# Optimization experiments

Hardware: AMD Instinct MI355X
Metric: run time of the kernel (lower is better)

The kernel has to match this reference:

```python
import jax, jax.numpy as jnp
import numpy as np

N_LAYERS = 11
DILATIONS = tuple(2 ** i for i in range(N_LAYERS))   # 1..1024
MEM_SIZES = DILATIONS                                 # kernel=2 -> 1 past tap -> mem = dilation
HOP = 128
C_SCALE = 1.0
FFT = 256       # channel width
NUM_CLS = 256   # mu-law classes
COND = 80       # mel bands
FRAMES = 16


def setup_inputs() -> dict:
    key = jax.random.key(0)
    ks = jax.random.split(key, 10)
    s = 0.05  # keep logits well-scaled for softmax sampling
    return {
        "y": jax.random.normal(ks[0], (COND, FRAMES), jnp.float32),
        "samples": jax.random.uniform(ks[1], (FRAMES * HOP,), jnp.float32),
        "emb_raw": jax.random.normal(ks[2], (NUM_CLS, FFT), jnp.float32) * 0.5,
        "condition_W": jax.random.normal(ks[3], (N_LAYERS * FFT, COND), jnp.float32) * s,
        "WV_past": jax.random.normal(ks[4], (N_LAYERS, FFT, FFT, 1), jnp.float32) * s,
        "WV_present": jax.random.normal(ks[5], (N_LAYERS, FFT, FFT), jnp.float32) * s,
        "W_o_w": jax.random.normal(ks[6], (N_LAYERS, FFT, FFT), jnp.float32) * s,
        "W_o_b": jax.random.normal(ks[7], (N_LAYERS, FFT), jnp.float32) * s,
        "end_w": jax.random.normal(ks[8], (NUM_CLS, FFT), jnp.float32) * s,
        "end_b": jax.random.normal(ks[9], (NUM_CLS,), jnp.float32) * s,
    }


def reference(y, samples, emb_raw, condition_W, WV_past, WV_present, W_o_w, W_o_b, end_w, end_b):
    emb = jnp.tanh(emb_raw)                      # fftnet.emb[0].weight.tanh()
    T = y.shape[1] * HOP
    # F.interpolate nearest with scale_factor=hop_length == frame repeat
    yu = jnp.repeat(y, HOP, axis=1)              # [COND, T]
    # precompute all conditioning projections (condition_W @ y[:, i], chunked per layer)
    conds = (condition_W @ yu).reshape(N_LAYERS, FFT, T).transpose(2, 0, 1)  # [T, L, FFT]

    bufs0 = tuple(jnp.zeros((FFT, m), jnp.float32) for m in MEM_SIZES)
    x0 = emb[NUM_CLS // 2 - 1]
    n_taps = WV_past.shape[3]

    def step(carry, inp):
        x, bufs = carry
        cond_t, u, t = inp
        new_bufs = []
        for j in range(N_LAYERS):
            mem = bufs[j]
            m = MEM_SIZES[j]
            idx = t % m                                   # ring-buffer write/oldest-read ptr
            h = cond_t[j]
            ii = idx
            for k in range(n_taps):                       # read past taps (before write)
                h = h + WV_past[j, :, :, k] @ mem[:, ii]
                ii = (ii + DILATIONS[j]) % m
            h = h + WV_present[j] @ x
            new_bufs.append(mem.at[:, idx].set(x))        # write current x into ring buffer
            h = jax.nn.relu(h)
            z = W_o_w[j] @ h + W_o_b[j]
            x = jax.nn.relu(z + x)                        # residual + relu
        logits = (end_w @ x + end_b) * C_SCALE
        cum = jnp.cumsum(jax.nn.softmax(logits))
        new_idx = jnp.argmax(cum > u)                     # nonzero(cum > u)[0]
        return (emb[new_idx], tuple(new_bufs)), new_idx

    ts = jnp.arange(T)
    _, outputs = jax.lax.scan(step, (x0, bufs0), (conds, samples, ts))
    return outputs  # [T] int sampled mu-law classes
```

## Files before the change

kernel.cpp:

```cpp
#include <hip/hip_runtime.h>
#include <math.h>


#define T_STEPS 2048
#define NROLE   32

typedef unsigned long long u64;
typedef float v64f __attribute__((ext_vector_type(64)));

#define OFF_EMBT   0
#define OFF_WPET   65536
#define OFF_WVPET  131072
#define OFF_RINGS  196608
#define OFF_TAPQ   1244672
#define OFF_ZQ     1408512
#define OFF_XQ     1419776
#define WS_FLOATS  1425408

#define FIDX     0
#define FBAR(r)  (32 + 32*(r))

__device__ __forceinline__ float ldc(const float* p) {
  int v = __hip_atomic_load((const int*)p, __ATOMIC_RELAXED, __HIP_MEMORY_SCOPE_AGENT);
  return __int_as_float(v);
}
__device__ __forceinline__ void stc(float* p, float x) {
  __hip_atomic_store((int*)p, __float_as_int(x), __ATOMIC_RELAXED, __HIP_MEMORY_SCOPE_AGENT);
}
__device__ __forceinline__ u64 ldq(const u64* p) {
  return __hip_atomic_load(p, __ATOMIC_RELAXED, __HIP_MEMORY_SCOPE_AGENT);
}
__device__ __forceinline__ void stq(u64* p, float v, int tag) {
  u64 x = (u64)(unsigned)__float_as_int(v) | ((u64)(unsigned)tag << 32);
  __hip_atomic_store(p, x, __ATOMIC_RELAXED, __HIP_MEMORY_SCOPE_AGENT);
}
__device__ __forceinline__ int ptag(u64 q) { return (int)(q >> 32); }
__device__ __forceinline__ float pval(u64 q) { return __int_as_float((int)(unsigned)q); }

__device__ __forceinline__ float spin_pair(const u64* p, int want) {
  int bud = 1 << 20; u64 q;
  do { q = ldq(p); } while (ptag(q) < want && --bud > 0);
  return pval(q);
}
__device__ __forceinline__ void spin3(const u64* p1, const u64* p2, const u64* p3,
                                      int want, float& v1, float& v2, float& v3) {
  int bud = 1 << 20; u64 q1, q2, q3; bool ok;
  do {
    q1 = ldq(p1); q2 = ldq(p2); q3 = ldq(p3);
    ok = (ptag(q1) >= want) & (ptag(q2) >= want) & (ptag(q3) >= want);
  } while (!ok && --bud > 0);
  v1 = pval(q1); v2 = pval(q2); v3 = pval(q3);
}
__device__ __forceinline__ void spin_tag2(const u64* p1, const u64* p2, int w1, int w2) {
  int bud = 1 << 20; u64 q1, q2; bool ok;
  do {
    q1 = ldq(p1); q2 = ldq(p2);
    ok = (ptag(q1) >= w1) & (ptag(q2) >= w2);
  } while (!ok && --bud > 0);
}
__device__ __forceinline__ void wait1(int* f, int want) {
  int it = 0;
  while (__hip_atomic_load(f, __ATOMIC_RELAXED, __HIP_MEMORY_SCOPE_AGENT) < want) {
    if (++it > (1 << 22)) break;
  }
  (void)__hip_atomic_load(f, __ATOMIC_ACQUIRE, __HIP_MEMORY_SCOPE_AGENT);
}
__device__ __forceinline__ void post(int* f, int v) {
  __hip_atomic_store(f, v, __ATOMIC_RELEASE, __HIP_MEMORY_SCOPE_AGENT);
}

__global__ __launch_bounds__(512, 1)
void fftnet_kernel(const float* __restrict__ y, const float* __restrict__ samples,
                   const float* __restrict__ emb_raw, const float* __restrict__ condW,
                   const float* __restrict__ WV_past, const float* __restrict__ WV_present,
                   const float* __restrict__ W_o_w, const float* __restrict__ W_o_b,
                   const float* __restrict__ end_w, const float* __restrict__ end_b,
                   int* __restrict__ out, float* __restrict__ ws)
{
  const int tid = threadIdx.x;
  const int role = blockIdx.x;
  int* iflags = (int*)(ws + WS_FLOATS);
  u64* zq  = (u64*)(ws + OFF_ZQ);
  u64* xq  = (u64*)(ws + OFF_XQ);
  u64* tq  = (u64*)(ws + OFF_TAPQ);

  __shared__ float s_x[256];
  __shared__ float s_h[256];
  __shared__ float s_p[1024];
  __shared__ float s_cond[16 * 256];
  __shared__ float s_tap[128];
  __shared__ float s_m[320];
  __shared__ unsigned long long s_mask[8];

  for (int i = role * 512 + tid; i < 65536; i += NROLE * 512)
    stc(ws + OFF_EMBT + i, tanhf(emb_raw[i]));
  __syncthreads();
  if (tid == 0) post(iflags + FBAR(role), 1);
  if (tid < NROLE) wait1(iflags + FBAR(tid), 1);
  __syncthreads();

  for (int n = role; n < 512; n += NROLE) {
    const float* wmat = (n < 256) ? WV_present : WV_past;
    int cls = n & 255;
    int c = tid & 255, s2 = tid >> 8;
    float acc = 0.f;
    for (int k = 128 * s2; k < 128 * s2 + 128; ++k)
      acc += wmat[c * 256 + k] * ws[OFF_EMBT + cls * 256 + k];
    s_p[s2 * 256 + c] = acc;
    __syncthreads();
    if (tid < 256)
      stc(ws + ((n < 256) ? OFF_WPET : OFF_WVPET) + cls * 256 + tid, s_p[tid] + s_p[256 + tid]);
    __syncthreads();
  }
  __syncthreads();
  if (tid == 0) post(iflags + FBAR(role), 2);
  if (tid < NROLE) wait1(iflags + FBAR(tid), 2);
  __syncthreads();
  __builtin_amdgcn_fence(__ATOMIC_ACQUIRE, "agent");
  __syncthreads();

  if (role == 0) {
    const int c = tid & 255, s2 = tid >> 8;
    v64f we0, we1;
#pragma unroll
    for (int i = 0; i < 64; ++i) we0[i] = end_w[c * 256 + 128 * s2 + i];
#pragma unroll
    for (int i = 0; i < 64; ++i) we1[i] = end_w[c * 256 + 128 * s2 + 64 + i];
    const float eb = end_b[c];
    const float b10 = W_o_b[10 * 256 + c];
    const u64* pza = zq + (10 * 2 + 0) * 256;
    const u64* pzb = zq + (10 * 2 + 1) * 256;
    const u64* pxq = xq + 10 * 256;
    const int lane = tid & 63, w = tid >> 6;
    if (tid == 0)
      __hip_atomic_store(iflags + FIDX, (1 << 8) | 127, __ATOMIC_RELAXED,
                         __HIP_MEMORY_SCOPE_AGENT);

    for (int t = 0; t < T_STEPS; ++t) {
      float u = samples[t];
      if (tid < 256) {
        float a, b, r3;
        spin3(pza + tid, pzb + tid, pxq + tid, t + 1, a, b, r3);
        s_x[tid] = fmaxf(a + b + b10 + r3, 0.f);
      }
      __syncthreads();
      float acc = 0.f;
#pragma unroll
      for (int i = 0; i < 64; ++i) acc += we0[i] * s_x[128 * s2 + i];
#pragma unroll
      for (int i = 0; i < 64; ++i) acc += we1[i] * s_x[128 * s2 + 64 + i];
      s_p[s2 * 256 + c] = acc;
      __syncthreads();
      float logit = 0.f;
      if (tid < 256) logit = s_p[tid] + s_p[256 + tid] + eb;
      float vmax = (tid < 256) ? logit : -3.4e38f;
#pragma unroll
      for (int d = 32; d > 0; d >>= 1) vmax = fmaxf(vmax, __shfl_xor(vmax, d, 64));
      if (lane == 0) s_m[280 + w] = vmax;
      __syncthreads();
      float mx = fmaxf(fmaxf(s_m[280], s_m[281]), fmaxf(s_m[282], s_m[283]));
      float e = (tid < 256) ? expf(logit - mx) : 0.f;
      float vs = e;
#pragma unroll
      for (int d = 32; d > 0; d >>= 1) vs += __shfl_xor(vs, d, 64);
      if (lane == 0) s_m[288 + w] = vs;
      __syncthreads();
      float ssum = s_m[288] + s_m[289] + s_m[290] + s_m[291];
      float p = (tid < 256) ? (e / ssum) : 0.f;
      float v = p;
#pragma unroll
      for (int d = 1; d < 64; d <<= 1) {
        float o = __shfl_up(v, (unsigned)d, 64);
        if (lane >= d) v += o;
      }
      if (tid < 256 && lane == 63) s_m[256 + w] = v;
      __syncthreads();
      float offs = 0.f;
      if (tid < 256) for (int k = 0; k < w; ++k) offs += s_m[256 + k];
      float cum = v + offs;
      unsigned long long msk = __ballot(tid < 256 && (cum > u));
      if (lane == 0) s_mask[w] = msk;
      __syncthreads();
      if (tid == 0) {
        int idx = 0;
        for (int k = 0; k < 4; ++k) {
          unsigned long long m2 = s_mask[k];
          if (m2) { idx = k * 64 + (int)__builtin_ctzll(m2); break; }
        }
        __hip_atomic_store(iflags + FIDX, ((t + 2) << 8) | idx, __ATOMIC_RELAXED,
                           __HIP_MEMORY_SCOPE_AGENT);
        out[t] = idx;
      }
      __syncthreads();
    }

  } else if (role == 1) {
    v64f wo00, wo01;
    { int c = tid & 255, s2 = tid >> 8;
#pragma unroll
      for (int i = 0; i < 64; ++i) wo00[i] = W_o_w[c * 256 + 128 * s2 + i];
#pragma unroll
      for (int i = 0; i < 64; ++i) wo01[i] = W_o_w[c * 256 + 128 * s2 + 64 + i]; }
    const float b0 = W_o_b[tid & 255];
    for (int e = tid; e < 4096; e += 512) {
      int f = e >> 8, r = e & 255;
      float a = 0.f;
      for (int q = 0; q < 80; ++q) a += condW[r * 80 + q] * y[q * 16 + f];
      s_cond[f * 256 + r] = a;
    }
    __syncthreads();
    u64* px1 = xq + 1 * 256;
    int pidx = 127;

    for (int t = 0; t < T_STEPS; ++t) {
      float tapv = 0.f;
      if (tid < 256 && t > 0) tapv = ws[OFF_WVPET + pidx * 256 + tid];
      int v, bud = 1 << 20;
      do {
        v = __hip_atomic_load(iflags + FIDX, __ATOMIC_RELAXED, __HIP_MEMORY_SCOPE_AGENT);
      } while (v < ((t + 1) << 8) && --bud > 0);
      const int idx = v & 255;
      if (tid < 256) {
        s_x[tid] = ws[OFF_EMBT + idx * 256 + tid];
        float hv = s_cond[(t >> 7) * 256 + tid] + ws[OFF_WPET + idx * 256 + tid] + tapv;
        s_h[tid] = fmaxf(hv, 0.f);
      }
      __syncthreads();
      {
        int c = tid & 255, s2 = tid >> 8;
        float a0 = 0.f, a1 = 0.f;
#pragma unroll
        for (int i = 0; i < 64; ++i) a0 += wo00[i] * s_h[128 * s2 + i];
#pragma unroll
        for (int i = 0; i < 64; ++i) a1 += wo01[i] * s_h[128 * s2 + 64 + i];
        s_p[s2 * 256 + c] = a0 + a1;
      }
      __syncthreads();
      if (tid < 256)
        stq(px1 + tid, fmaxf(s_p[tid] + s_p[256 + tid] + b0 + s_x[tid], 0.f), t + 1);
      pidx = idx;
    }

  } else if (role <= 21) {
    const int jj = (role <= 11) ? (role - 1) : (role - 11);
    const int side = (role <= 11) ? 0 : 1;
    const int base = side * 128;
    v64f wpv, wov;
    { const float* W = WV_present + jj * 65536;
      int r = tid & 127, s = tid >> 7;
#pragma unroll
      for (int i = 0; i < 64; ++i) wpv[i] = W[(base + r) * 256 + 64 * s + i]; }
    { const float* W = W_o_w + jj * 65536;
      int c = tid & 255, s2 = tid >> 8;
#pragma unroll
      for (int i = 0; i < 64; ++i) wov[i] = W[c * 256 + base + 64 * s2 + i]; }
    const float bprev = W_o_b[(jj - 1) * 256 + (tid & 255)];
    for (int e = tid; e < 2048; e += 512) {
      int f = e >> 7, rr = e & 127;
      float a = 0.f;
      for (int q = 0; q < 80; ++q) a += condW[(jj * 256 + base + rr) * 80 + q] * y[q * 16 + f];
      s_cond[f * 128 + rr] = a;
    }
    __syncthreads();
    const int dj = 1 << jj, maskj = 2 * dj - 1;
    float* ringj = ws + OFF_RINGS + 512 * (dj - 1);
    const u64* pza = zq + ((jj - 1) * 2 + 0) * 256;
    const u64* pzb = zq + ((jj - 1) * 2 + 1) * 256;
    const u64* pxp = xq + (jj - 1) * 256;
    u64* zout = zq + (jj * 2 + side) * 256;
    u64* xout = xq + jj * 256;
    const u64* ptap = tq + (jj - 1) * 32 * 256;

    for (int t = 0; t < T_STEPS; ++t) {
      const int want = t + 1;
      if (tid < 256) {
        float xv;
        if (jj == 1) {
          xv = spin_pair(xq + 1 * 256 + tid, want);
        } else {
          float a, b, r3;
          spin3(pza + tid, pzb + tid, pxp + tid, want, a, b, r3);
          xv = fmaxf(a + b + bprev + r3, 0.f);
        }
        s_x[tid] = xv;
        if (side == 0) {
          stc(ringj + (t & maskj) * 256 + tid, xv);
          if (jj >= 2) stq(xout + tid, xv, want);
        }
      } else if (tid < 384) {
        int l = tid - 256;
        s_tap[l] = spin_pair(ptap + (t & 31) * 256 + base + l, want);
      }
      __syncthreads();
      { int r = tid & 127, s = tid >> 7;
        float acc = 0.f;
#pragma unroll
        for (int i = 0; i < 64; ++i) acc += wpv[i] * s_x[64 * s + i];
        s_p[s * 128 + r] = acc; }
      __syncthreads();
      if (tid < 128) {
        int f = t >> 7;
        float hv = s_p[tid] + s_p[128 + tid] + s_p[256 + tid] + s_p[384 + tid]
                 + s_cond[f * 128 + tid] + s_tap[tid];
        s_h[tid] = fmaxf(hv, 0.f);
      }
      __syncthreads();
      { int cc = tid & 255, s2 = tid >> 8;
        float acc = 0.f;
#pragma unroll
        for (int i = 0; i < 64; ++i) acc += wov[i] * s_h[64 * s2 + i];
        s_p[s2 * 256 + cc] = acc; }
      __syncthreads();
      if (side == 0)
        __builtin_amdgcn_fence(__ATOMIC_RELEASE, "agent");
      if (tid < 256) stq(zout + tid, s_p[tid] + s_p[256 + tid], want);
    }

  } else {
    const int j = role - 21;
    const int dj = 1 << j, maskj = 2 * dj - 1;
    v64f wq0, wq1;
    { const float* W = WV_past + j * 65536;
      int r = tid & 255, s2 = tid >> 8;
#pragma unroll
      for (int i = 0; i < 64; ++i) wq0[i] = W[r * 256 + 128 * s2 + i];
#pragma unroll
      for (int i = 0; i < 64; ++i) wq1[i] = W[r * 256 + 128 * s2 + 64 + i]; }
    float* ringj = ws + OFF_RINGS + 512 * (dj - 1);
    u64* tapj = tq + (j - 1) * 32 * 256;
    const u64* pza = zq + (j * 2 + 0) * 256;
    const u64* pzb = zq + (j * 2 + 1) * 256;

    for (int t = 0; t < T_STEPS; ++t) {
      int wgA = (t >= dj) ? (t - dj + 1) : (t - 31);
      if (wgA < t - 31) wgA = t - 31;
      int wgB = t - 31;
      if (tid < 256 && (wgA >= 1 || wgB >= 1))
        spin_tag2(pza + tid, pzb + tid, wgA, wgB);
      float tapv = 0.f;
      if (t >= dj) {
        if (tid < 256) s_x[tid] = ldc(ringj + ((t - dj) & maskj) * 256 + tid);
        __syncthreads();
        int r = tid & 255, s2 = tid >> 8;
        float acc = 0.f;
#pragma unroll
        for (int i = 0; i < 64; ++i) acc += wq0[i] * s_x[128 * s2 + i];
#pragma unroll
        for (int i = 0; i < 64; ++i) acc += wq1[i] * s_x[128 * s2 + 64 + i];
        s_p[s2 * 256 + r] = acc;
        __syncthreads();
        if (tid < 256) tapv = s_p[tid] + s_p[256 + tid];
      }
      if (tid < 256) stq(tapj + (t & 31) * 256 + tid, tapv, t + 1);
      __syncthreads();
    }
  }
}

extern "C" void kernel_launch(void* const* d_in, const int* in_sizes, int n_in,
                              void* d_out, int out_size, void* d_ws, size_t ws_size,
                              hipStream_t stream) {
  const float* y       = (const float*)d_in[0];
  const float* samples = (const float*)d_in[1];
  const float* emb_raw = (const float*)d_in[2];
  const float* condW   = (const float*)d_in[3];
  const float* WV_past = (const float*)d_in[4];
  const float* WV_pres = (const float*)d_in[5];
  const float* W_o_w   = (const float*)d_in[6];
  const float* W_o_b   = (const float*)d_in[7];
  const float* end_w   = (const float*)d_in[8];
  const float* end_b   = (const float*)d_in[9];
  (void)in_sizes; (void)n_in; (void)out_size; (void)ws_size;
  hipLaunchKernelGGL(fftnet_kernel, dim3(NROLE), dim3(512), 0, stream,
                     y, samples, emb_raw, condW, WV_past, WV_pres,
                     W_o_w, W_o_b, end_w, end_b, (int*)d_out, (float*)d_ws);
}
```

Baseline: 55.18 ms.

## Split each layer across four blocks and fuse layer-0 output into layer-1 blocks

Raises the persistent grid from 32 to 53 blocks so that each residual layer's present-matvec and output-projection is split four ways across blocks instead of two, and each produces a quarter of the z partial sums. Layer 0 becomes two blocks that publish only z partials, and layer 1 computes x from those plus the embedding and the sampled index, which is now published through a tagged 64-bit queue. The aim is to shorten the per-step serial critical path by doing less work per block per layer. In exchange, every consumer must spin on more flag words, and inter-block traffic grows.

```diff
diff --git a/kernel.cpp b/kernel.cpp
--- a/kernel.cpp
+++ b/kernel.cpp
@@ -3,7 +3,7 @@
 
 
 #define T_STEPS 2048
-#define NROLE   32
+#define NBLK    53
 
 typedef unsigned long long u64;
 typedef float v64f __attribute__((ext_vector_type(64)));
@@ -13,12 +13,12 @@
 #define OFF_WVPET  131072
 #define OFF_RINGS  196608
 #define OFF_TAPQ   1244672
-#define OFF_ZQ     1408512
-#define OFF_XQ     1419776
-#define WS_FLOATS  1425408
-
-#define FIDX     0
-#define FBAR(r)  (32 + 32*(r))
+#define OFF_ZQ4    1408512
+#define OFF_XQ     1431040
+#define OFF_IDXQ   1436672
+#define WS_FLOATS  1436736
+
+#define FBAR(r)  (32*(r))
 
 __device__ __forceinline__ float ldc(const float* p) {
   int v = __hip_atomic_load((const int*)p, __ATOMIC_RELAXED, __HIP_MEMORY_SCOPE_AGENT);
@@ -41,6 +41,11 @@
   int bud = 1 << 20; u64 q;
   do { q = ldq(p); } while (ptag(q) < want && --bud > 0);
   return pval(q);
+}
+__device__ __forceinline__ int spin_idx(const u64* p, int want) {
+  int bud = 1 << 20; u64 q;
+  do { q = ldq(p); } while (ptag(q) < want && --bud > 0);
+  return __float_as_int(pval(q)) & 255;
 }
 __device__ __forceinline__ void spin3(const u64* p1, const u64* p2, const u64* p3,
                                       int want, float& v1, float& v2, float& v3) {
@@ -50,6 +55,17 @@
     ok = (ptag(q1) >= want) & (ptag(q2) >= want) & (ptag(q3) >= want);
   } while (!ok && --bud > 0);
   v1 = pval(q1); v2 = pval(q2); v3 = pval(q3);
+}
+__device__ __forceinline__ void spin5(const u64* p0, const u64* p1, const u64* p2,
+                                      const u64* p3, const u64* p4, int want,
+                                      float& v0, float& v1, float& v2, float& v3, float& v4) {
+  int bud = 1 << 20; u64 q0, q1, q2, q3, q4; bool ok;
+  do {
+    q0 = ldq(p0); q1 = ldq(p1); q2 = ldq(p2); q3 = ldq(p3); q4 = ldq(p4);
+    ok = (ptag(q0) >= want) & (ptag(q1) >= want) & (ptag(q2) >= want)
+       & (ptag(q3) >= want) & (ptag(q4) >= want);
+  } while (!ok && --bud > 0);
+  v0 = pval(q0); v1 = pval(q1); v2 = pval(q2); v3 = pval(q3); v4 = pval(q4);
 }
 __device__ __forceinline__ void spin_tag2(const u64* p1, const u64* p2, int w1, int w2) {
   int bud = 1 << 20; u64 q1, q2; bool ok;
@@ -78,28 +94,29 @@
                    int* __restrict__ out, float* __restrict__ ws)
 {
   const int tid = threadIdx.x;
-  const int role = blockIdx.x;
+  const int bid = blockIdx.x;
   int* iflags = (int*)(ws + WS_FLOATS);
-  u64* zq  = (u64*)(ws + OFF_ZQ);
-  u64* xq  = (u64*)(ws + OFF_XQ);
-  u64* tq  = (u64*)(ws + OFF_TAPQ);
+  u64* zq4  = (u64*)(ws + OFF_ZQ4);
+  u64* xq   = (u64*)(ws + OFF_XQ);
+  u64* tq   = (u64*)(ws + OFF_TAPQ);
+  u64* idxq = (u64*)(ws + OFF_IDXQ);
 
   __shared__ float s_x[256];
   __shared__ float s_h[256];
   __shared__ float s_p[1024];
-  __shared__ float s_cond[16 * 256];
-  __shared__ float s_tap[128];
+  __shared__ float s_cond[2048];
+  __shared__ float s_tap[64];
   __shared__ float s_m[320];
   __shared__ unsigned long long s_mask[8];
 
-  for (int i = role * 512 + tid; i < 65536; i += NROLE * 512)
+  for (int i = bid * 512 + tid; i < 65536; i += NBLK * 512)
     stc(ws + OFF_EMBT + i, tanhf(emb_raw[i]));
   __syncthreads();
-  if (tid == 0) post(iflags + FBAR(role), 1);
-  if (tid < NROLE) wait1(iflags + FBAR(tid), 1);
-  __syncthreads();
-
-  for (int n = role; n < 512; n += NROLE) {
+  if (tid == 0) post(iflags + FBAR(bid), 1);
+  if (tid < NBLK) wait1(iflags + FBAR(tid), 1);
+  __syncthreads();
+
+  for (int n = bid; n < 512; n += NBLK) {
     const float* wmat = (n < 256) ? WV_present : WV_past;
     int cls = n & 255;
     int c = tid & 255, s2 = tid >> 8;
@@ -113,13 +130,13 @@
     __syncthreads();
   }
   __syncthreads();
-  if (tid == 0) post(iflags + FBAR(role), 2);
-  if (tid < NROLE) wait1(iflags + FBAR(tid), 2);
+  if (tid == 0) post(iflags + FBAR(bid), 2);
+  if (tid < NBLK) wait1(iflags + FBAR(tid), 2);
   __syncthreads();
   __builtin_amdgcn_fence(__ATOMIC_ACQUIRE, "agent");
   __syncthreads();
 
-  if (role == 0) {
+  if (bid == 0) {
     const int c = tid & 255, s2 = tid >> 8;
     v64f we0, we1;
 #pragma unroll
@@ -128,20 +145,21 @@
     for (int i = 0; i < 64; ++i) we1[i] = end_w[c * 256 + 128 * s2 + 64 + i];
     const float eb = end_b[c];
     const float b10 = W_o_b[10 * 256 + c];
-    const u64* pza = zq + (10 * 2 + 0) * 256;
-    const u64* pzb = zq + (10 * 2 + 1) * 256;
+    const u64* pz0 = zq4 + (10 * 4 + 0) * 256;
+    const u64* pz1 = zq4 + (10 * 4 + 1) * 256;
+    const u64* pz2 = zq4 + (10 * 4 + 2) * 256;
+    const u64* pz3 = zq4 + (10 * 4 + 3) * 256;
     const u64* pxq = xq + 10 * 256;
     const int lane = tid & 63, w = tid >> 6;
-    if (tid == 0)
-      __hip_atomic_store(iflags + FIDX, (1 << 8) | 127, __ATOMIC_RELAXED,
-                         __HIP_MEMORY_SCOPE_AGENT);
+    if (tid == 0) stq(idxq, __int_as_float(127), 1);
 
     for (int t = 0; t < T_STEPS; ++t) {
       float u = samples[t];
       if (tid < 256) {
-        float a, b, r3;
-        spin3(pza + tid, pzb + tid, pxq + tid, t + 1, a, b, r3);
-        s_x[tid] = fmaxf(a + b + b10 + r3, 0.f);
+        float a, b, cc, d, r3;
+        spin5(pz0 + tid, pz1 + tid, pz2 + tid, pz3 + tid, pxq + tid, t + 1, a, b, cc, d, r3);
+        float s01 = a + b, s23 = cc + d;
+        s_x[tid] = fmaxf(s01 + s23 + b10 + r3, 0.f);
       }
       __syncthreads();
       float acc = 0.f;
@@ -155,23 +173,23 @@
       if (tid < 256) logit = s_p[tid] + s_p[256 + tid] + eb;
       float vmax = (tid < 256) ? logit : -3.4e38f;
 #pragma unroll
-      for (int d = 32; d > 0; d >>= 1) vmax = fmaxf(vmax, __shfl_xor(vmax, d, 64));
+      for (int d2 = 32; d2 > 0; d2 >>= 1) vmax = fmaxf(vmax, __shfl_xor(vmax, d2, 64));
       if (lane == 0) s_m[280 + w] = vmax;
       __syncthreads();
       float mx = fmaxf(fmaxf(s_m[280], s_m[281]), fmaxf(s_m[282], s_m[283]));
       float e = (tid < 256) ? expf(logit - mx) : 0.f;
       float vs = e;
 #pragma unroll
-      for (int d = 32; d > 0; d >>= 1) vs += __shfl_xor(vs, d, 64);
+      for (int d2 = 32; d2 > 0; d2 >>= 1) vs += __shfl_xor(vs, d2, 64);
       if (lane == 0) s_m[288 + w] = vs;
       __syncthreads();
       float ssum = s_m[288] + s_m[289] + s_m[290] + s_m[291];
       float p = (tid < 256) ? (e / ssum) : 0.f;
       float v = p;
 #pragma unroll
-      for (int d = 1; d < 64; d <<= 1) {
-        float o = __shfl_up(v, (unsigned)d, 64);
-        if (lane >= d) v += o;
+      for (int d2 = 1; d2 < 64; d2 <<= 1) {
+        float o = __shfl_up(v, (unsigned)d2, 64);
+        if (lane >= d2) v += o;
       }
       if (tid < 256 && lane == 63) s_m[256 + w] = v;
       __syncthreads();
@@ -187,87 +205,82 @@
           unsigned long long m2 = s_mask[k];
           if (m2) { idx = k * 64 + (int)__builtin_ctzll(m2); break; }
         }
-        __hip_atomic_store(iflags + FIDX, ((t + 2) << 8) | idx, __ATOMIC_RELAXED,
-                           __HIP_MEMORY_SCOPE_AGENT);
+        stq(idxq, __int_as_float(idx), t + 2);
         out[t] = idx;
       }
       __syncthreads();
     }
 
-  } else if (role == 1) {
-    v64f wo00, wo01;
-    { int c = tid & 255, s2 = tid >> 8;
-#pragma unroll
-      for (int i = 0; i < 64; ++i) wo00[i] = W_o_w[c * 256 + 128 * s2 + i];
-#pragma unroll
-      for (int i = 0; i < 64; ++i) wo01[i] = W_o_w[c * 256 + 128 * s2 + 64 + i]; }
-    const float b0 = W_o_b[tid & 255];
-    for (int e = tid; e < 4096; e += 512) {
-      int f = e >> 8, r = e & 255;
-      float a = 0.f;
-      for (int q = 0; q < 80; ++q) a += condW[r * 80 + q] * y[q * 16 + f];
-      s_cond[f * 256 + r] = a;
-    }
-    __syncthreads();
-    u64* px1 = xq + 1 * 256;
-    int pidx = 127;
-
-    for (int t = 0; t < T_STEPS; ++t) {
-      float tapv = 0.f;
-      if (tid < 256 && t > 0) tapv = ws[OFF_WVPET + pidx * 256 + tid];
-      int v, bud = 1 << 20;
-      do {
-        v = __hip_atomic_load(iflags + FIDX, __ATOMIC_RELAXED, __HIP_MEMORY_SCOPE_AGENT);
-      } while (v < ((t + 1) << 8) && --bud > 0);
-      const int idx = v & 255;
-      if (tid < 256) {
-        s_x[tid] = ws[OFF_EMBT + idx * 256 + tid];
-        float hv = s_cond[(t >> 7) * 256 + tid] + ws[OFF_WPET + idx * 256 + tid] + tapv;
-        s_h[tid] = fmaxf(hv, 0.f);
-      }
-      __syncthreads();
-      {
-        int c = tid & 255, s2 = tid >> 8;
-        float a0 = 0.f, a1 = 0.f;
-#pragma unroll
-        for (int i = 0; i < 64; ++i) a0 += wo00[i] * s_h[128 * s2 + i];
-#pragma unroll
-        for (int i = 0; i < 64; ++i) a1 += wo01[i] * s_h[128 * s2 + 64 + i];
-        s_p[s2 * 256 + c] = a0 + a1;
-      }
-      __syncthreads();
-      if (tid < 256)
-        stq(px1 + tid, fmaxf(s_p[tid] + s_p[256 + tid] + b0 + s_x[tid], 0.f), t + 1);
-      pidx = idx;
-    }
-
-  } else if (role <= 21) {
-    const int jj = (role <= 11) ? (role - 1) : (role - 11);
-    const int side = (role <= 11) ? 0 : 1;
-    const int base = side * 128;
-    v64f wpv, wov;
-    { const float* W = WV_present + jj * 65536;
-      int r = tid & 127, s = tid >> 7;
-#pragma unroll
-      for (int i = 0; i < 64; ++i) wpv[i] = W[(base + r) * 256 + 64 * s + i]; }
-    { const float* W = W_o_w + jj * 65536;
-      int c = tid & 255, s2 = tid >> 8;
-#pragma unroll
-      for (int i = 0; i < 64; ++i) wov[i] = W[c * 256 + base + 64 * s2 + i]; }
-    const float bprev = W_o_b[(jj - 1) * 256 + (tid & 255)];
+  } else if (bid <= 2) {
+    const int side = bid - 1;
+    const int row = tid & 255, chunk = tid >> 8;
+    v64f wv;
+#pragma unroll
+    for (int i = 0; i < 64; ++i)
+      wv[i] = W_o_w[row * 256 + side * 128 + chunk * 64 + i];
     for (int e = tid; e < 2048; e += 512) {
       int f = e >> 7, rr = e & 127;
       float a = 0.f;
-      for (int q = 0; q < 80; ++q) a += condW[(jj * 256 + base + rr) * 80 + q] * y[q * 16 + f];
+      for (int q = 0; q < 80; ++q) a += condW[(side * 128 + rr) * 80 + q] * y[q * 16 + f];
       s_cond[f * 128 + rr] = a;
+    }
+    __syncthreads();
+    u64* zout = zq4 + (0 * 4 + side) * 256;
+    int pidx = 127;
+
+    for (int t = 0; t < T_STEPS; ++t) {
+      int idx = pidx;
+      if (tid < 128) {
+        float tapv = (t > 0) ? ws[OFF_WVPET + pidx * 256 + side * 128 + tid] : 0.f;
+        idx = spin_idx(idxq, t + 1);
+        float hv = s_cond[(t >> 7) * 128 + tid]
+                 + ws[OFF_WPET + idx * 256 + side * 128 + tid] + tapv;
+        s_h[tid] = fmaxf(hv, 0.f);
+        if (tid == 0) s_m[300] = __int_as_float(idx);
+      }
+      __syncthreads();
+      float acc = 0.f;
+#pragma unroll
+      for (int i = 0; i < 64; ++i) acc += wv[i] * s_h[64 * chunk + i];
+      s_p[chunk * 256 + row] = acc;
+      __syncthreads();
+      if (tid < 256) stq(zout + tid, s_p[tid] + s_p[256 + tid], t + 1);
+      pidx = (tid < 128) ? idx : __float_as_int(s_m[300]);
+      __syncthreads();
+    }
+
+  } else if (bid <= 42) {
+    const int jj = 1 + ((bid - 3) >> 2);
+    const int k  = (bid - 3) & 3;
+    v64f wv;
+    if (tid < 256) {
+      int r = tid & 63, s = tid >> 6;
+#pragma unroll
+      for (int i = 0; i < 64; ++i)
+        wv[i] = WV_present[jj * 65536 + (64 * k + r) * 256 + 64 * s + i];
+    } else {
+      int row = tid - 256;
+#pragma unroll
+      for (int i = 0; i < 64; ++i)
+        wv[i] = W_o_w[jj * 65536 + row * 256 + 64 * k + i];
+    }
+    const float bprev = W_o_b[(jj - 1) * 256 + (tid & 255)];
+    for (int e = tid; e < 1024; e += 512) {
+      int f = e >> 6, rr = e & 63;
+      float a = 0.f;
+      for (int q = 0; q < 80; ++q)
+        a += condW[(jj * 256 + 64 * k + rr) * 80 + q] * y[q * 16 + f];
+      s_cond[f * 64 + rr] = a;
     }
     __syncthreads();
     const int dj = 1 << jj, maskj = 2 * dj - 1;
     float* ringj = ws + OFF_RINGS + 512 * (dj - 1);
-    const u64* pza = zq + ((jj - 1) * 2 + 0) * 256;
-    const u64* pzb = zq + ((jj - 1) * 2 + 1) * 256;
+    const u64* pz0 = zq4 + ((jj - 1) * 4 + 0) * 256;
+    const u64* pz1 = zq4 + ((jj - 1) * 4 + 1) * 256;
+    const u64* pz2 = zq4 + ((jj - 1) * 4 + 2) * 256;
+    const u64* pz3 = zq4 + ((jj - 1) * 4 + 3) * 256;
     const u64* pxp = xq + (jj - 1) * 256;
-    u64* zout = zq + (jj * 2 + side) * 256;
+    u64* zout = zq4 + (jj * 4 + k) * 256;
     u64* xout = xq + jj * 256;
     const u64* ptap = tq + (jj - 1) * 32 * 256;
 
@@ -276,67 +289,73 @@
       if (tid < 256) {
         float xv;
         if (jj == 1) {
-          xv = spin_pair(xq + 1 * 256 + tid, want);
+          float a, b, iv;
+          spin3(pz0 + tid, pz1 + tid, idxq, want, a, b, iv);
+          int idx = __float_as_int(iv) & 255;
+          xv = fmaxf((a + b) + bprev + ws[OFF_EMBT + idx * 256 + tid], 0.f);
         } else {
-          float a, b, r3;
-          spin3(pza + tid, pzb + tid, pxp + tid, want, a, b, r3);
-          xv = fmaxf(a + b + bprev + r3, 0.f);
+          float a, b, cc, d, xp;
+          spin5(pz0 + tid, pz1 + tid, pz2 + tid, pz3 + tid, pxp + tid, want, a, b, cc, d, xp);
+          float s01 = a + b, s23 = cc + d;
+          xv = fmaxf(s01 + s23 + bprev + xp, 0.f);
         }
         s_x[tid] = xv;
-        if (side == 0) {
-          stc(ringj + (t & maskj) * 256 + tid, xv);
-          if (jj >= 2) stq(xout + tid, xv, want);
-        }
-      } else if (tid < 384) {
-        int l = tid - 256;
-        s_tap[l] = spin_pair(ptap + (t & 31) * 256 + base + l, want);
-      }
-      __syncthreads();
-      { int r = tid & 127, s = tid >> 7;
+        if (k == 0) stq(xout + tid, xv, want);
+      } else if (tid >= 384 && tid < 448) {
+        int l = tid - 384;
+        s_tap[l] = spin_pair(ptap + (t & 31) * 256 + 64 * k + l, want);
+      }
+      __syncthreads();
+      if (tid < 256) {
+        int r = tid & 63, s = tid >> 6;
         float acc = 0.f;
 #pragma unroll
-        for (int i = 0; i < 64; ++i) acc += wpv[i] * s_x[64 * s + i];
-        s_p[s * 128 + r] = acc; }
-      __syncthreads();
-      if (tid < 128) {
-        int f = t >> 7;
-        float hv = s_p[tid] + s_p[128 + tid] + s_p[256 + tid] + s_p[384 + tid]
-                 + s_cond[f * 128 + tid] + s_tap[tid];
+        for (int i = 0; i < 64; ++i) acc += wv[i] * s_x[64 * s + i];
+        s_p[s * 64 + r] = acc;
+      } else if (k == 0) {
+        int row = tid - 256;
+        stc(ringj + (t & maskj) * 256 + row, s_x[row]);
+      }
+      __syncthreads();
+      if (tid < 64) {
+        float hv = s_p[tid] + s_p[64 + tid] + s_p[128 + tid] + s_p[192 + tid]
+                 + s_cond[(t >> 7) * 64 + tid] + s_tap[tid];
         s_h[tid] = fmaxf(hv, 0.f);
       }
       __syncthreads();
-      { int cc = tid & 255, s2 = tid >> 8;
+      if (tid >= 256) {
+        int row = tid - 256;
         float acc = 0.f;
 #pragma unroll
-        for (int i = 0; i < 64; ++i) acc += wov[i] * s_h[64 * s2 + i];
-        s_p[s2 * 256 + cc] = acc; }
-      __syncthreads();
-      if (side == 0)
-        __builtin_amdgcn_fence(__ATOMIC_RELEASE, "agent");
-      if (tid < 256) stq(zout + tid, s_p[tid] + s_p[256 + tid], want);
+        for (int i = 0; i < 64; ++i) acc += wv[i] * s_h[i];
+        if (k == 0)
+          __builtin_amdgcn_fence(__ATOMIC_RELEASE, "agent");
+        stq(zout + row, acc, want);
+      }
+      __syncthreads();
     }
 
   } else {
-    const int j = role - 21;
+    const int j = bid - 42;
     const int dj = 1 << j, maskj = 2 * dj - 1;
     v64f wq0, wq1;
-    { const float* W = WV_past + j * 65536;
-      int r = tid & 255, s2 = tid >> 8;
-#pragma unroll
-      for (int i = 0; i < 64; ++i) wq0[i] = W[r * 256 + 128 * s2 + i];
-#pragma unroll
-      for (int i = 0; i < 64; ++i) wq1[i] = W[r * 256 + 128 * s2 + 64 + i]; }
+    { int r = tid & 255, s2 = tid >> 8;
+#pragma unroll
+      for (int i = 0; i < 64; ++i) wq0[i] = WV_past[j * 65536 + r * 256 + 128 * s2 + i];
+#pragma unroll
+      for (int i = 0; i < 64; ++i) wq1[i] = WV_past[j * 65536 + r * 256 + 128 * s2 + 64 + i]; }
     float* ringj = ws + OFF_RINGS + 512 * (dj - 1);
     u64* tapj = tq + (j - 1) * 32 * 256;
-    const u64* pza = zq + (j * 2 + 0) * 256;
-    const u64* pzb = zq + (j * 2 + 1) * 256;
+    const u64* z0 = zq4 + (j * 4 + 0) * 256;
 
     for (int t = 0; t < T_STEPS; ++t) {
-      int wgA = (t >= dj) ? (t - dj + 1) : (t - 31);
-      if (wgA < t - 31) wgA = t - 31;
-      int wgB = t - 31;
-      if (tid < 256 && (wgA >= 1 || wgB >= 1))
-        spin_tag2(pza + tid, pzb + tid, wgA, wgB);
+      int g0 = t - 31;
+      if (t >= dj && t - dj + 1 > g0) g0 = t - dj + 1;
+      int gk = t - 31;
+      if (tid < 256 && (g0 >= 1 || gk >= 1)) {
+        const u64* zk = zq4 + (j * 4 + (tid >> 6)) * 256;
+        spin_tag2(z0 + tid, zk + tid, g0, gk);
+      }
       float tapv = 0.f;
       if (t >= dj) {
         if (tid < 256) s_x[tid] = ldc(ringj + ((t - dj) & maskj) * 256 + tid);
@@ -371,7 +390,7 @@
   const float* end_w   = (const float*)d_in[8];
   const float* end_b   = (const float*)d_in[9];
   (void)in_sizes; (void)n_in; (void)out_size; (void)ws_size;
-  hipLaunchKernelGGL(fftnet_kernel, dim3(NROLE), dim3(512), 0, stream,
+  hipLaunchKernelGGL(fftnet_kernel, dim3(NBLK), dim3(512), 0, stream,
                      y, samples, emb_raw, condW, WV_past, WV_pres,
                      W_o_w, W_o_b, end_w, end_b, (int*)d_out, (float*)d_ws);
 }
```

Result: faster. 50.48 ms (-8.5%).
